# Performance work log

Hardware: AMD Instinct MI355X
Metric: run time of the kernel (lower is better)

The kernel has to match this reference:

```python
import jax, jax.numpy as jnp
import numpy as np

B, T = 32, 2048            # batch, seq_len
V = 16                     # vocab_size
H = 256                    # hidden_size
NV = V + 2                 # embedding rows (padding_idx=0 + vocab + delimiter)
NO = V + 1                 # head output size


def setup_inputs() -> dict:
    key = jax.random.key(0)
    ks = jax.random.split(key, 8)
    s = 1.0 / np.sqrt(H).astype(np.float32)
    tokens = jax.random.randint(ks[0], (B, T), 0, NV)
    embed = jax.random.normal(ks[1], (NV, H), jnp.float32) * 0.02
    embed = embed.at[0].set(0.0)  # padding_idx=0
    # GRU params (PyTorch layout: gates [r|z|n] stacked on last dim)
    W_ih = jax.random.uniform(ks[2], (H, 3 * H), jnp.float32, -s, s)
    W_hh = jax.random.uniform(ks[3], (H, 3 * H), jnp.float32, -s, s)
    b_ih = jax.random.uniform(ks[4], (3 * H,), jnp.float32, -s, s)
    b_hh = jax.random.uniform(ks[5], (3 * H,), jnp.float32, -s, s)
    W_head = jax.random.uniform(ks[6], (H, NO), jnp.float32, -s, s)
    b_head = jax.random.uniform(ks[7], (NO,), jnp.float32, -s, s)
    return {"tokens": tokens, "embed": embed, "W_ih": W_ih, "W_hh": W_hh,
            "b_ih": b_ih, "b_hh": b_hh, "W_head": W_head, "b_head": b_head}


def _mogru_scan(x, W_ih, W_hh, b_ih, b_hh):
    # x: [B, T, H]. Precompute all input projections in one big GEMM.
    gi = x @ W_ih + b_ih                      # [B, T, 3H]
    gi_t = jnp.swapaxes(gi, 0, 1)             # [T, B, 3H] for scan
    h0 = jnp.zeros((x.shape[0], W_hh.shape[0]), x.dtype)

    def step(h, gi_step):
        gh = h @ W_hh + b_hh                  # [B, 3H]
        i_r, i_z, i_n = jnp.split(gi_step, 3, axis=-1)
        h_r, h_z, h_n = jnp.split(gh, 3, axis=-1)
        r = jax.nn.sigmoid(i_r + h_r)
        z = jax.nn.sigmoid(i_z + h_z)         # beta: retention gate
        n = jnp.tanh(i_n + r * h_n)
        h_new = (1.0 - z) * n + z * h
        return h_new, (h_new, z)

    h_last, (outs, betas) = jax.lax.scan(step, h0, gi_t)
    return jnp.swapaxes(outs, 0, 1), h_last, jnp.swapaxes(betas, 0, 1)


def reference(tokens, embed, W_ih, W_hh, b_ih, b_hh, W_head, b_head):
    x = embed[tokens]                          # [B, T, H] embedding lookup
    output, _, betas = _mogru_scan(x, W_ih, W_hh, b_ih, b_hh)
    logits = output @ W_head + b_head          # [B, T, V+1]
    return logits, betas
```

## Files before the change

kernel.cpp:

```cpp
#include <hip/hip_runtime.h>

#define BB   32
#define TT   2048
#define HH   256
#define G3   768
#define NVOC 18
#define NOUT 17
#define LOGITS_ELEMS ((size_t)BB * TT * NOUT)

typedef _Float16 h2 __attribute__((ext_vector_type(2)));

__device__ __forceinline__ float bf1(unsigned short u){
  union{unsigned int i; float f;} v; v.i = ((unsigned int)u) << 16; return v.f;
}
__device__ __forceinline__ unsigned short f2bf(float f){
  union{float f; unsigned int i;} v; v.f = f;
  unsigned int lsb = (v.i >> 16) & 1u;
  v.i += 0x7fffu + lsb;
  return (unsigned short)(v.i >> 16);
}

__device__ __forceinline__ float ld1(const float* p, size_t i){ return p[i]; }
__device__ __forceinline__ float ld1(const unsigned short* p, size_t i){ return bf1(p[i]); }

__device__ __forceinline__ bool detect_f32(const void* W_ih_raw){
  const unsigned short* u = (const unsigned short*)W_ih_raw;
  bool big = false;
  #pragma unroll
  for (int i = 0; i < 64; i++){
    float v = bf1(u[i]);
    big |= !(v >= -0.25f && v <= 0.25f);
  }
  return big;
}

#if __has_builtin(__builtin_amdgcn_fdot2)
#define FDOT2(a,b,c) __builtin_amdgcn_fdot2((a),(b),(c),false)
#else
#define FDOT2(a,b,c) ((c) + (float)(a).x*(float)(b).x + (float)(a).y*(float)(b).y)
#endif

__device__ __forceinline__ h2 bch2(unsigned int u){ return __builtin_bit_cast(h2, u); }
__device__ __forceinline__ h2 bch2f(float f){ return __builtin_bit_cast(h2, f); }

__device__ __forceinline__ float pair_swap(float v){
  int i = __builtin_bit_cast(int, v);
  i = __builtin_amdgcn_mov_dpp(i, 0xB1, 0xF, 0xF, true);
  return __builtin_bit_cast(float, i);
}

__device__ __forceinline__ void bar_lds(){
  asm volatile("s_waitcnt lgkmcnt(0)\n\ts_barrier" ::: "memory");
}

template<typename T>
__device__ __forceinline__ void prep_body(const T* W_hh, float4* Wp4){
  int s   = blockIdx.x * 256 + threadIdx.x;
  int tid = s & 511;
  int jg  = s >> 9;
  int p   = tid >> 1, q = tid & 1;
  int g   = jg >> 4,  jx = jg & 15;
  int col = (g << 8) + p;
  int k0  = (q << 7) + (jx << 3);
  float c0, c1, c2, c3;
  #pragma unroll
  for (int c = 0; c < 4; c++){
    h2 pr;
    pr.x = (_Float16)ld1(W_hh, (size_t)(k0 + 2*c    ) * G3 + col);
    pr.y = (_Float16)ld1(W_hh, (size_t)(k0 + 2*c + 1) * G3 + col);
    float fc = __builtin_bit_cast(float, pr);
    if (c == 0) c0 = fc; else if (c == 1) c1 = fc;
    else if (c == 2) c2 = fc; else c3 = fc;
  }
  float4 v; v.x = c0; v.y = c1; v.z = c2; v.w = c3;
  Wp4[s] = v;
}

__global__ __launch_bounds__(256) void k_prep(
    const void* __restrict__ W_hh, const void* __restrict__ W_ih,
    float4* __restrict__ Wp4)
{
  if (detect_f32(W_ih)) prep_body<float>((const float*)W_hh, Wp4);
  else                  prep_body<unsigned short>((const unsigned short*)W_hh, Wp4);
}

template<typename T>
__device__ __forceinline__ void proj_body(const T* embed, const T* W_ih,
                                          const T* b_ih, const T* b_hh,
                                          float* proj, float* bb){
  __shared__ float s_e[HH];
  int v = blockIdx.x, j = threadIdx.x;
  if (j < HH) s_e[j] = ld1(embed, (size_t)v * HH + j);
  if (v == 0) bb[j] = ld1(b_hh, (size_t)j);
  __syncthreads();
  float acc = ld1(b_ih, (size_t)j);
  #pragma unroll 8
  for (int k = 0; k < HH; k++)
    acc += s_e[k] * ld1(W_ih, (size_t)k * G3 + j);
  proj[(size_t)v * G3 + j] = acc;
}

__global__ __launch_bounds__(768) void k_proj(
    const void* __restrict__ embed, const void* __restrict__ W_ih,
    const void* __restrict__ b_ih, const void* __restrict__ b_hh,
    float* __restrict__ proj, float* __restrict__ bb)
{
  if (detect_f32(W_ih))
    proj_body<float>((const float*)embed, (const float*)W_ih,
                     (const float*)b_ih, (const float*)b_hh, proj, bb);
  else
    proj_body<unsigned short>((const unsigned short*)embed,
                              (const unsigned short*)W_ih,
                              (const unsigned short*)b_ih,
                              (const unsigned short*)b_hh, proj, bb);
}

__global__ __launch_bounds__(512, 2) void k_scan(
    const int*    __restrict__ tokens,
    const float4* __restrict__ Wp4,
    const float*  __restrict__ bb,
    const void*   __restrict__ W_ih,
    const float*  __restrict__ proj,
    _Float16*     __restrict__ outs,
    void*         __restrict__ d_out_base)
{
  __shared__ float s_proj[NVOC * G3];
  __shared__ int   s_tok[TT];
  __shared__ __align__(16) _Float16 s_h[2][HH];

  const bool f32m = detect_f32(W_ih);
  const int b   = blockIdx.x;
  const int tid = threadIdx.x;
  const int p   = tid >> 1;
  const int q   = tid & 1;

  for (int i = tid; i < NVOC * G3 / 4; i += 512)
    ((float4*)s_proj)[i] = ((const float4*)proj)[i];
  ((int4*)s_tok)[tid] = ((const int4*)(tokens + (size_t)b * TT))[tid];

  float4 wreg[48];
  {
    const float4* wp = Wp4 + tid;
    #pragma unroll
    for (int i = 0; i < 48; i++) wreg[i] = wp[(size_t)i * 512];
  }
  const float bhr = bb[p];
  const float bhz = bb[HH + p];
  const float bhn = bb[2*HH + p];

  if (tid < HH) s_h[0][tid] = (_Float16)0.f;
  float h_old = 0.f;

  _Float16*       orow   = outs + (size_t)b * TT * HH + p;
  unsigned short* brow_b = (unsigned short*)d_out_base + LOGITS_ELEMS
                           + (size_t)b * TT * HH + p;
  float*          brow_f = (float*)d_out_base + LOGITS_ELEMS
                           + (size_t)b * TT * HH + p;

  __syncthreads();

  for (int t = 0; t < TT; t++) {
    int tok = s_tok[t];
    const float* pj = s_proj + tok * G3;
    float gir = pj[p];
    float giz = pj[HH + p];
    float gin = pj[2*HH + p];

    const int4* hb = (const int4*)(&s_h[t & 1][0]) + (q << 4);

    float r0=0.f,r1=0.f,r2=0.f,r3=0.f;
    float z0=0.f,z1=0.f,z2=0.f,z3=0.f;
    float n0=0.f,n1=0.f,n2=0.f,n3=0.f;
    #pragma unroll
    for (int jx = 0; jx < 16; jx++) {
      int4 hv = hb[jx];
      h2 x0 = bch2((unsigned)hv.x);
      h2 x1 = bch2((unsigned)hv.y);
      h2 x2 = bch2((unsigned)hv.z);
      h2 x3 = bch2((unsigned)hv.w);
      float4 wr = wreg[jx];
      float4 wz = wreg[16 + jx];
      float4 wn = wreg[32 + jx];
      r0 = FDOT2(bch2f(wr.x), x0, r0);
      r1 = FDOT2(bch2f(wr.y), x1, r1);
      r2 = FDOT2(bch2f(wr.z), x2, r2);
      r3 = FDOT2(bch2f(wr.w), x3, r3);
      z0 = FDOT2(bch2f(wz.x), x0, z0);
      z1 = FDOT2(bch2f(wz.y), x1, z1);
      z2 = FDOT2(bch2f(wz.z), x2, z2);
      z3 = FDOT2(bch2f(wz.w), x3, z3);
      n0 = FDOT2(bch2f(wn.x), x0, n0);
      n1 = FDOT2(bch2f(wn.y), x1, n1);
      n2 = FDOT2(bch2f(wn.z), x2, n2);
      n3 = FDOT2(bch2f(wn.w), x3, n3);
    }
    float ghr = (r0 + r1) + (r2 + r3);
    float ghz = (z0 + z1) + (z2 + z3);
    float ghn = (n0 + n1) + (n2 + n3);
    ghr += pair_swap(ghr);
    ghz += pair_swap(ghz);
    ghn += pair_swap(ghn);
    ghr += bhr; ghz += bhz; ghn += bhn;

    float r = 1.f / (1.f + __expf(-(gir + ghr)));
    float z = 1.f / (1.f + __expf(-(giz + ghz)));
    float x = gin + r * ghn;
    x = fminf(fmaxf(x, -15.f), 15.f);
    float e = __expf(2.f * x);
    float n = (e - 1.f) / (e + 1.f);
    float hn = (1.f - z) * n + z * h_old;
    h_old = hn;

    if (q == 0) {
      s_h[(t + 1) & 1][p] = (_Float16)hn;
      orow[(size_t)t * HH] = (_Float16)hn;
    } else {
      if (f32m) brow_f[(size_t)t * HH] = z;
      else      brow_b[(size_t)t * HH] = f2bf(z);
    }
    bar_lds();
  }
}

#define WSTR 129

template<typename T>
__device__ __forceinline__ void stage_head(const T* W_head, const T* b_head,
                                           h2* s_w, float* s_b, int tid){
  for (int i = tid; i < NOUT * 128; i += 256) {
    int o = i >> 7, ip = i & 127;
    h2 pr;
    pr.x = (_Float16)ld1(W_head, (size_t)(2*ip    ) * NOUT + o);
    pr.y = (_Float16)ld1(W_head, (size_t)(2*ip + 1) * NOUT + o);
    s_w[o * WSTR + ip] = pr;
  }
  if (tid < NOUT) s_b[tid] = ld1(b_head, (size_t)tid);
}

__global__ __launch_bounds__(256) void k_head(
    const _Float16* __restrict__ outs,
    const void* __restrict__ W_head,
    const void* __restrict__ b_head,
    const void* __restrict__ W_ih,
    void* __restrict__ logits_out)
{
  __shared__ h2 s_w[NOUT * WSTR];
  __shared__ float s_b[NOUT];
  const bool f32m = detect_f32(W_ih);
  const int tid = threadIdx.x;

  if (f32m) stage_head<float>((const float*)W_head, (const float*)b_head,
                              s_w, s_b, tid);
  else      stage_head<unsigned short>((const unsigned short*)W_head,
                                       (const unsigned short*)b_head,
                                       s_w, s_b, tid);
  __syncthreads();

  size_t gid = (size_t)blockIdx.x * 256 + tid;
  if (gid >= LOGITS_ELEMS) return;
  int o = (int)(gid % NOUT);
  size_t row = gid / NOUT;

  const uint4* xp = (const uint4*)(outs + row * HH);
  const h2* wv = s_w + o * WSTR;
  float a0 = 0.f, a1 = 0.f, a2 = 0.f, a3 = 0.f;
  #pragma unroll 8
  for (int kk = 0; kk < 32; kk++) {
    uint4 u = xp[kk];
    int kb = kk * 4;
    a0 = FDOT2(bch2(u.x), wv[kb+0], a0);
    a1 = FDOT2(bch2(u.y), wv[kb+1], a1);
    a2 = FDOT2(bch2(u.z), wv[kb+2], a2);
    a3 = FDOT2(bch2(u.w), wv[kb+3], a3);
  }
  float val = ((a0 + a1) + (a2 + a3)) + s_b[o];
  if (f32m) ((float*)logits_out)[gid] = val;
  else      ((unsigned short*)logits_out)[gid] = f2bf(val);
}

extern "C" void kernel_launch(void* const* d_in, const int* in_sizes, int n_in,
                              void* d_out, int out_size, void* d_ws, size_t ws_size,
                              hipStream_t stream)
{
  const int* tokens = (const int*)d_in[0];
  const void* embed  = d_in[1];
  const void* W_ih   = d_in[2];
  const void* W_hh   = d_in[3];
  const void* b_ih   = d_in[4];
  const void* b_hh   = d_in[5];
  const void* W_head = d_in[6];
  const void* b_head = d_in[7];

  char* ws = (char*)d_ws;
  float*    proj = (float*)ws;
  float*    bb   = (float*)(ws + 55296);
  float4*   Wp4  = (float4*)(ws + 55296 + 3072);
  _Float16* outs = (_Float16*)(ws + 55296 + 3072 + 393216);

  k_prep<<<96, 256, 0, stream>>>(W_hh, W_ih, Wp4);
  k_proj<<<NVOC, G3, 0, stream>>>(embed, W_ih, b_ih, b_hh, proj, bb);
  k_scan<<<BB, 512, 0, stream>>>(tokens, Wp4, bb, W_ih, proj, outs, d_out);
  k_head<<<(int)((LOGITS_ELEMS + 255) / 256), 256, 0, stream>>>(
      outs, W_head, b_head, W_ih, d_out);
}
```

Baseline: 2.651 ms.

## Remap GRU scan lanes to 4-lane groups computing two hidden units each

Each group of four lanes now computes two hidden units, with every lane covering a quarter of the K dimension. Partial sums are combined with two DPP steps (quad swap and pair swap). The hidden state in LDS is stored in a swizzled layout and read with XOR-permuted indices to avoid bank conflicts. Output and beta stores are packed as 2-element words, and the weight registers are declared as named scalars through macros rather than an array. The goal is fewer LDS reads per lane, fewer bank conflicts and fewer store instructions in the serial recurrence loop, at the cost of more intricate indexing and a risk of mismatching the prep layout.

```diff
diff --git a/kernel.cpp b/kernel.cpp
--- a/kernel.cpp
+++ b/kernel.cpp
@@ -43,9 +43,14 @@
 __device__ __forceinline__ h2 bch2(unsigned int u){ return __builtin_bit_cast(h2, u); }
 __device__ __forceinline__ h2 bch2f(float f){ return __builtin_bit_cast(h2, f); }
 
-__device__ __forceinline__ float pair_swap(float v){
+__device__ __forceinline__ float dppB1(float v){
   int i = __builtin_bit_cast(int, v);
   i = __builtin_amdgcn_mov_dpp(i, 0xB1, 0xF, 0xF, true);
+  return __builtin_bit_cast(float, i);
+}
+__device__ __forceinline__ float dpp4E(float v){
+  int i = __builtin_bit_cast(int, v);
+  i = __builtin_amdgcn_mov_dpp(i, 0x4E, 0xF, 0xF, true);
   return __builtin_bit_cast(float, i);
 }
 
@@ -57,11 +62,12 @@
 __device__ __forceinline__ void prep_body(const T* W_hh, float4* Wp4){
   int s   = blockIdx.x * 256 + threadIdx.x;
   int tid = s & 511;
-  int jg  = s >> 9;
-  int p   = tid >> 1, q = tid & 1;
-  int g   = jg >> 4,  jx = jg & 15;
-  int col = (g << 8) + p;
-  int k0  = (q << 7) + (jx << 3);
+  int r9  = s >> 9;
+  int jx  = r9 & 7, gi = r9 >> 3;
+  int g   = gi >> 1, ii = gi & 1;
+  int a   = tid >> 2, lq = tid & 3;
+  int col = (g << 8) + (a << 1) + ii;
+  int k0  = (lq << 6) + (jx << 3);
   float c0, c1, c2, c3;
   #pragma unroll
   for (int c = 0; c < 4; c++){
@@ -115,6 +121,45 @@
                               (const unsigned short*)b_hh, proj, bb);
 }
 
+
+#define FORJX(M, g, i, base) \
+  M(g,i,0,(base)+0) M(g,i,1,(base)+1) M(g,i,2,(base)+2) M(g,i,3,(base)+3) \
+  M(g,i,4,(base)+4) M(g,i,5,(base)+5) M(g,i,6,(base)+6) M(g,i,7,(base)+7)
+#define FORALLW(M) \
+  FORJX(M,r,0,0)  FORJX(M,r,1,8)  FORJX(M,z,0,16) \
+  FORJX(M,z,1,24) FORJX(M,n,0,32) FORJX(M,n,1,40)
+
+#define DECLW(g,i,jx,idx) float4 w_##g##i##_##jx = wp[(idx)*512];
+
+#define DOTJ(jx) { \
+  int4 hv = hp[hix##jx]; \
+  h2 x0 = bch2((unsigned)hv.x), x1 = bch2((unsigned)hv.y), \
+     x2 = bch2((unsigned)hv.z), x3 = bch2((unsigned)hv.w); \
+  ar0 = FDOT2(bch2f(w_r0_##jx.x), x0, ar0); \
+  ar1 = FDOT2(bch2f(w_r1_##jx.x), x0, ar1); \
+  az0 = FDOT2(bch2f(w_z0_##jx.x), x0, az0); \
+  az1 = FDOT2(bch2f(w_z1_##jx.x), x0, az1); \
+  an0 = FDOT2(bch2f(w_n0_##jx.x), x0, an0); \
+  an1 = FDOT2(bch2f(w_n1_##jx.x), x0, an1); \
+  ar0 = FDOT2(bch2f(w_r0_##jx.y), x1, ar0); \
+  ar1 = FDOT2(bch2f(w_r1_##jx.y), x1, ar1); \
+  az0 = FDOT2(bch2f(w_z0_##jx.y), x1, az0); \
+  az1 = FDOT2(bch2f(w_z1_##jx.y), x1, az1); \
+  an0 = FDOT2(bch2f(w_n0_##jx.y), x1, an0); \
+  an1 = FDOT2(bch2f(w_n1_##jx.y), x1, an1); \
+  ar0 = FDOT2(bch2f(w_r0_##jx.z), x2, ar0); \
+  ar1 = FDOT2(bch2f(w_r1_##jx.z), x2, ar1); \
+  az0 = FDOT2(bch2f(w_z0_##jx.z), x2, az0); \
+  az1 = FDOT2(bch2f(w_z1_##jx.z), x2, az1); \
+  an0 = FDOT2(bch2f(w_n0_##jx.z), x2, an0); \
+  an1 = FDOT2(bch2f(w_n1_##jx.z), x2, an1); \
+  ar0 = FDOT2(bch2f(w_r0_##jx.w), x3, ar0); \
+  ar1 = FDOT2(bch2f(w_r1_##jx.w), x3, ar1); \
+  az0 = FDOT2(bch2f(w_z0_##jx.w), x3, az0); \
+  az1 = FDOT2(bch2f(w_z1_##jx.w), x3, az1); \
+  an0 = FDOT2(bch2f(w_n0_##jx.w), x3, an0); \
+  an1 = FDOT2(bch2f(w_n1_##jx.w), x3, an1); }
+
 __global__ __launch_bounds__(512, 2) void k_scan(
     const int*    __restrict__ tokens,
     const float4* __restrict__ Wp4,
@@ -131,92 +176,84 @@
   const bool f32m = detect_f32(W_ih);
   const int b   = blockIdx.x;
   const int tid = threadIdx.x;
-  const int p   = tid >> 1;
-  const int q   = tid & 1;
+  const int a   = tid >> 2;
+  const int lq  = tid & 3;
+  const int sel = lq >> 1;
+  const int u   = 2*a + sel;
 
   for (int i = tid; i < NVOC * G3 / 4; i += 512)
     ((float4*)s_proj)[i] = ((const float4*)proj)[i];
   ((int4*)s_tok)[tid] = ((const int4*)(tokens + (size_t)b * TT))[tid];
-
-  float4 wreg[48];
+  if (tid < 256) ((int*)s_h)[tid] = 0;
+
+  const float4* wp = Wp4 + tid;
+  FORALLW(DECLW)
+
+  const float bhr = bb[u];
+  const float bhz = bb[HH + u];
+  const float bhn = bb[2*HH + u];
+
+  int pa;
   {
-    const float4* wp = Wp4 + tid;
-    #pragma unroll
-    for (int i = 0; i < 48; i++) wreg[i] = wp[(size_t)i * 512];
-  }
-  const float bhr = bb[p];
-  const float bhz = bb[HH + p];
-  const float bhn = bb[2*HH + p];
-
-  if (tid < HH) s_h[0][tid] = (_Float16)0.f;
+    int Ld = a >> 2, md = a >> 5;
+    pa = (((Ld & 24) | ((Ld & 7) ^ md)) << 2) | (a & 3);
+  }
+  const int hb = lq << 3;
+  const int hix0 = hb | (0 ^ lq), hix1 = hb | (1 ^ lq), hix2 = hb | (2 ^ lq),
+            hix3 = hb | (3 ^ lq), hix4 = hb | (4 ^ lq), hix5 = hb | (5 ^ lq),
+            hix6 = hb | (6 ^ lq), hix7 = hb | (7 ^ lq);
+
   float h_old = 0.f;
 
-  _Float16*       orow   = outs + (size_t)b * TT * HH + p;
-  unsigned short* brow_b = (unsigned short*)d_out_base + LOGITS_ELEMS
-                           + (size_t)b * TT * HH + p;
-  float*          brow_f = (float*)d_out_base + LOGITS_ELEMS
-                           + (size_t)b * TT * HH + p;
+  unsigned* orow_u = (unsigned*)outs + (((size_t)b * TT * HH) >> 1) + a;
+  unsigned* brow_u = (unsigned*)((unsigned short*)d_out_base + LOGITS_ELEMS)
+                     + (((size_t)b * TT * HH) >> 1) + a;
+  float2*   brow_f = (float2*)((float*)d_out_base + LOGITS_ELEMS)
+                     + (((size_t)b * TT * HH) >> 1) + a;
 
   __syncthreads();
 
   for (int t = 0; t < TT; t++) {
     int tok = s_tok[t];
     const float* pj = s_proj + tok * G3;
-    float gir = pj[p];
-    float giz = pj[HH + p];
-    float gin = pj[2*HH + p];
-
-    const int4* hb = (const int4*)(&s_h[t & 1][0]) + (q << 4);
-
-    float r0=0.f,r1=0.f,r2=0.f,r3=0.f;
-    float z0=0.f,z1=0.f,z2=0.f,z3=0.f;
-    float n0=0.f,n1=0.f,n2=0.f,n3=0.f;
-    #pragma unroll
-    for (int jx = 0; jx < 16; jx++) {
-      int4 hv = hb[jx];
-      h2 x0 = bch2((unsigned)hv.x);
-      h2 x1 = bch2((unsigned)hv.y);
-      h2 x2 = bch2((unsigned)hv.z);
-      h2 x3 = bch2((unsigned)hv.w);
-      float4 wr = wreg[jx];
-      float4 wz = wreg[16 + jx];
-      float4 wn = wreg[32 + jx];
-      r0 = FDOT2(bch2f(wr.x), x0, r0);
-      r1 = FDOT2(bch2f(wr.y), x1, r1);
-      r2 = FDOT2(bch2f(wr.z), x2, r2);
-      r3 = FDOT2(bch2f(wr.w), x3, r3);
-      z0 = FDOT2(bch2f(wz.x), x0, z0);
-      z1 = FDOT2(bch2f(wz.y), x1, z1);
-      z2 = FDOT2(bch2f(wz.z), x2, z2);
-      z3 = FDOT2(bch2f(wz.w), x3, z3);
-      n0 = FDOT2(bch2f(wn.x), x0, n0);
-      n1 = FDOT2(bch2f(wn.y), x1, n1);
-      n2 = FDOT2(bch2f(wn.z), x2, n2);
-      n3 = FDOT2(bch2f(wn.w), x3, n3);
-    }
-    float ghr = (r0 + r1) + (r2 + r3);
-    float ghz = (z0 + z1) + (z2 + z3);
-    float ghn = (n0 + n1) + (n2 + n3);
-    ghr += pair_swap(ghr);
-    ghz += pair_swap(ghz);
-    ghn += pair_swap(ghn);
-    ghr += bhr; ghz += bhz; ghn += bhn;
-
-    float r = 1.f / (1.f + __expf(-(gir + ghr)));
-    float z = 1.f / (1.f + __expf(-(giz + ghz)));
-    float x = gin + r * ghn;
+    float gir = pj[u];
+    float giz = pj[HH + u];
+    float gin = pj[2*HH + u];
+
+    const int4* hp = (const int4*)(&s_h[t & 1][0]);
+
+    float ar0=0.f, ar1=0.f, az0=0.f, az1=0.f, an0=0.f, an1=0.f;
+    DOTJ(0) DOTJ(1) DOTJ(2) DOTJ(3) DOTJ(4) DOTJ(5) DOTJ(6) DOTJ(7)
+
+    float pr = sel ? ar1 : ar0,  qr = sel ? ar0 : ar1;
+    float pz = sel ? az1 : az0,  qz = sel ? az0 : az1;
+    float pn = sel ? an1 : an0,  qn = sel ? an0 : an1;
+    pr += dpp4E(qr);  pz += dpp4E(qz);  pn += dpp4E(qn);
+    pr += dppB1(pr);  pz += dppB1(pz);  pn += dppB1(pn);
+
+    float r = 1.f / (1.f + __expf(-(gir + pr + bhr)));
+    float z = 1.f / (1.f + __expf(-(giz + pz + bhz)));
+    float x = gin + r * (pn + bhn);
     x = fminf(fmaxf(x, -15.f), 15.f);
     float e = __expf(2.f * x);
     float n = (e - 1.f) / (e + 1.f);
     float hn = (1.f - z) * n + z * h_old;
     h_old = hn;
 
-    if (q == 0) {
-      s_h[(t + 1) & 1][p] = (_Float16)hn;
-      orow[(size_t)t * HH] = (_Float16)hn;
-    } else {
-      if (f32m) brow_f[(size_t)t * HH] = z;
-      else      brow_b[(size_t)t * HH] = f2bf(z);
+    float hn_o = dpp4E(hn);
+    float z_o  = dpp4E(z);
+
+    if (lq == 0) {
+      h2 ph; ph.x = (_Float16)hn; ph.y = (_Float16)hn_o;
+      ((unsigned*)(&s_h[(t + 1) & 1][0]))[pa] = __builtin_bit_cast(unsigned, ph);
+    } else if (lq == 2) {
+      h2 po; po.x = (_Float16)hn_o; po.y = (_Float16)hn;
+      orow_u[(size_t)t * (HH/2)] = __builtin_bit_cast(unsigned, po);
+    } else if (lq == 1) {
+      if (f32m) { float2 fz; fz.x = z; fz.y = z_o;
+                  brow_f[(size_t)t * (HH/2)] = fz; }
+      else      { unsigned pz2 = (unsigned)f2bf(z) | ((unsigned)f2bf(z_o) << 16);
+                  brow_u[(size_t)t * (HH/2)] = pz2; }
     }
     bar_lds();
   }
```

Measured after the change: 2.617 ms. Within noise of the previous version (-1.3%).
